# Optimization experiments

Measured on AMD Instinct MI355X. Metric: run time of the kernel, lower is better.

## Reference

```python
import jax, jax.numpy as jnp
import numpy as np

B, A, STATE_LEN, H, REL_LEN, E = 32, 64, 256, 128, 64, 16

def _mlp2(x, w1, b1, w2, b2):
    # DI-engine MLP, 2 layers, ReLU after every layer (incl. output)
    return jax.nn.relu(jax.nn.relu(x @ w1 + b1) @ w2 + b2)

def setup_inputs() -> dict:
    key = jax.random.key(0)
    ks = jax.random.split(key, 16)
    def w(k, fi, fo):
        return (jax.random.normal(k, (fi, fo), jnp.float32) / np.float32(np.sqrt(fi)))
    z = lambda n: jnp.zeros((n,), jnp.float32)
    return {
        "states": jax.random.normal(ks[0], (B, A, STATE_LEN), jnp.float32),
        "relations": jax.random.normal(ks[1], (B, A, A, REL_LEN), jnp.float32),
        "alive_mask": (jax.random.uniform(ks[2], (B, A)) > 0.3).astype(jnp.float32),
        "se_w1": w(ks[3], STATE_LEN, H), "se_b1": z(H),
        "se_w2": w(ks[4], H, H), "se_b2": z(H),
        "re_w1": w(ks[5], H + REL_LEN, H), "re_b1": z(H),
        "re_w2": w(ks[6], H, 2 * H), "re_b2": z(2 * H),
        "ra_w": w(ks[7], 3 * H, H), "ra_b": z(H),
        "ae_w1": w(ks[8], 4 * H, H), "ae_b1": z(H),
        "ae_w2": w(ks[9], H, 2 * H), "ae_b2": z(2 * H),
        "action_embed": jax.random.normal(ks[10], (E, H), jnp.float32) * np.float32(np.sqrt(2.0 / H)),
        "action_mask": jnp.ones((B, A, E + A), jnp.int32),
        "action": jax.random.randint(ks[11], (B,), 0, E + A),
        "agent_id": 0,
    }

def reference(states, relations, alive_mask,
              se_w1, se_b1, se_w2, se_b2,
              re_w1, re_b1, re_w2, re_b2,
              ra_w, ra_b,
              ae_w1, ae_b1, ae_w2, ae_b2,
              action_embed, action_mask, action, agent_id):
    del action_mask  # read by the torch module but never used
    b, a = states.shape[0], states.shape[1]
    h, e = se_w2.shape[1], action_embed.shape[0]
    # encode per-agent state: [B,A,H]
    s = _mlp2(states, se_w1, se_b1, se_w2, se_b2)
    # relation encoder: concat target-agent state onto each relation edge
    rel_in = jnp.concatenate(
        [relations, jnp.broadcast_to(s[:, None], (b, a, a, h))], axis=-1)
    r = _mlp2(rel_in, re_w1, re_b1, re_w2, re_b2)               # [B,A,A,2H]
    # relation aggregator: masked mean / masked max over source agents
    r_avr, r_max = jnp.split(r, 2, axis=-1)
    m = alive_mask[:, None, :, None]                             # [B,1,A,1]
    r_avr = (r_avr * m).mean(axis=-2)                            # [B,A,H]
    r_max = (r_max * m).max(axis=-2)                             # [B,A,H]
    s = jax.nn.relu(jnp.concatenate([s, r_avr, r_max], axis=-1) @ ra_w + ra_b)
    # pairwise action embeddings: [B,A,A,2H]
    ae_in = jnp.concatenate(
        [r,
         jnp.broadcast_to(s[:, None], (b, a, a, h)),
         jnp.broadcast_to(s[:, :, None], (b, a, a, h))], axis=-1)
    ae = _mlp2(ae_in, ae_w1, ae_b1, ae_w2, ae_b2)
    active, passive = jnp.split(ae, 2, axis=-1)                  # [B,A,A,H] each
    # acting agent `agent_id`: candidates = [embed_num self actions | A targeted actions]
    active_i = active[:, agent_id]                               # [B,A,H]
    active_full = jnp.concatenate(
        [jnp.broadcast_to(action_embed[None], (b, e, h)), active_i], axis=1)  # [B,E+A,H]
    sel = jnp.take_along_axis(active_full, action[:, None, None], axis=1)     # [B,1,H]
    state = s.at[:, agent_id].add(sel[:, 0])
    # passive side: target j receives passive embed iff action == E + j, else zero
    passive_i = passive[:, agent_id]                             # [B,A,H]
    hit = (action[:, None] == (e + jnp.arange(a))[None, :])      # [B,A]
    passive_sel = jnp.where(hit[:, :, None], passive_i, jnp.zeros((), states.dtype))
    state = state + passive_sel
    return state, sel[:, :, None], passive_sel
```

## Files before the change

### kernel.cpp

```cpp
#include <hip/hip_runtime.h>

#define NB 32
#define NA 64
#define SLEN 256
#define NH 128
#define RLEN 64
#define NE 16

typedef _Float16 f16;
typedef _Float16 f16x8 __attribute__((ext_vector_type(8)));
typedef _Float16 f16x4 __attribute__((ext_vector_type(4)));
typedef float f32x4 __attribute__((ext_vector_type(4)));

__device__ inline f16x8 cvt8(float4 a, float4 b) {
  f16x8 r;
  r[0] = (f16)a.x; r[1] = (f16)a.y; r[2] = (f16)a.z; r[3] = (f16)a.w;
  r[4] = (f16)b.x; r[5] = (f16)b.y; r[6] = (f16)b.z; r[7] = (f16)b.w;
  return r;
}

__global__ __launch_bounds__(256) void k0_pack(const float* __restrict__ re_w1,
                                               const float* __restrict__ re_w2,
                                               const float* __restrict__ se_w1,
                                               const float* __restrict__ se_w2,
                                               const float* __restrict__ ra_w,
                                               const float* __restrict__ ae_w1,
                                               const float* __restrict__ ae_w2,
                                               f16* __restrict__ pk) {
  int idx = blockIdx.x * 256 + threadIdx.x;
  const float* src;
  int ro, N, ld, base;
  if (idx < 8192)        { src = re_w1; ro = 0;   N = 128; ld = 128; base = 0; }
  else if (idx < 40960)  { src = re_w2; ro = 0;   N = 256; ld = 256; base = 8192; }
  else if (idx < 73728)  { src = se_w1; ro = 0;   N = 128; ld = 128; base = 40960; }
  else if (idx < 90112)  { src = se_w2; ro = 0;   N = 128; ld = 128; base = 73728; }
  else if (idx < 106496) { src = re_w1; ro = 64;  N = 128; ld = 128; base = 90112; }
  else if (idx < 155648) { src = ra_w;  ro = 0;   N = 128; ld = 128; base = 106496; }
  else if (idx < 172032) { src = ae_w1; ro = 256; N = 128; ld = 128; base = 155648; }
  else if (idx < 188416) { src = ae_w1; ro = 384; N = 128; ld = 128; base = 172032; }
  else if (idx < 221184) { src = ae_w1; ro = 0;   N = 128; ld = 128; base = 188416; }
  else if (idx < 253952) { src = ae_w2; ro = 0;   N = 256; ld = 256; base = 221184; }
  else return;
  int li = idx - base;
  int t = li & 7, l = (li >> 3) & 63, rem = li >> 9;
  int NT = N >> 4;
  int nt = rem % NT, kt = rem / NT;
  int k = kt * 32 + (l >> 4) * 8 + t;
  int n = nt * 16 + (l & 15);
  pk[idx] = (f16)src[(size_t)(ro + k) * ld + n];
}

__global__ __launch_bounds__(256) void k1m(const float* __restrict__ states,
                                           const float* __restrict__ se_b1,
                                           const float* __restrict__ se_b2,
                                           const float* __restrict__ re_b1,
                                           const f16* __restrict__ pse1,
                                           const f16* __restrict__ pse2,
                                           const f16* __restrict__ pre1b,
                                           float* __restrict__ s_out,
                                           float* __restrict__ sp_pk) {
  __shared__ f16 t1[16 * 128];
  __shared__ f16 t2[16 * 128];
  const int row0 = blockIdx.x * 16;
  const int tid = threadIdx.x;
  const int w = tid >> 6, l = tid & 63, lr = l & 15, lh = l >> 4;

  f32x4 acc[2];
  acc[0] = (f32x4){0.f, 0.f, 0.f, 0.f};
  acc[1] = (f32x4){0.f, 0.f, 0.f, 0.f};

#pragma unroll
  for (int kt = 0; kt < 8; ++kt) {
    const float* p = states + (size_t)(row0 + lr) * SLEN + kt * 32 + lh * 8;
    f16x8 aF = cvt8(*(const float4*)p, *(const float4*)(p + 4));
#pragma unroll
    for (int n = 0; n < 2; ++n) {
      f16x8 bF = *(const f16x8*)(pse1 + ((size_t)(kt * 8 + w * 2 + n) * 64 + l) * 8);
      acc[n] = __builtin_amdgcn_mfma_f32_16x16x32_f16(aF, bF, acc[n], 0, 0, 0);
    }
  }
#pragma unroll
  for (int n = 0; n < 2; ++n) {
    int h = w * 32 + n * 16 + lr;
    float bias = se_b1[h];
#pragma unroll
    for (int reg = 0; reg < 4; ++reg) {
      int j = lh * 4 + reg;
      float v = fmaxf(acc[n][reg] + bias, 0.f);
      unsigned off = (unsigned)((j * NH + h) * 2) ^ ((unsigned)(j & 7) << 4);
      *(f16*)((char*)t1 + off) = (f16)v;
    }
  }
  __syncthreads();

  acc[0] = (f32x4){0.f, 0.f, 0.f, 0.f};
  acc[1] = (f32x4){0.f, 0.f, 0.f, 0.f};
#pragma unroll
  for (int kt = 0; kt < 4; ++kt) {
    unsigned off = (unsigned)((lr * NH + kt * 32 + lh * 8) * 2) ^ ((unsigned)(lr & 7) << 4);
    f16x8 aF = *(const f16x8*)((char*)t1 + off);
#pragma unroll
    for (int n = 0; n < 2; ++n) {
      f16x8 bF = *(const f16x8*)(pse2 + ((size_t)(kt * 8 + w * 2 + n) * 64 + l) * 8);
      acc[n] = __builtin_amdgcn_mfma_f32_16x16x32_f16(aF, bF, acc[n], 0, 0, 0);
    }
  }
#pragma unroll
  for (int n = 0; n < 2; ++n) {
    int h = w * 32 + n * 16 + lr;
    float bias = se_b2[h];
#pragma unroll
    for (int reg = 0; reg < 4; ++reg) {
      int j = lh * 4 + reg;
      float v = fmaxf(acc[n][reg] + bias, 0.f);
      s_out[(size_t)(row0 + j) * NH + h] = v;
      unsigned off = (unsigned)((j * NH + h) * 2) ^ ((unsigned)(j & 7) << 4);
      *(f16*)((char*)t2 + off) = (f16)v;
    }
  }
  __syncthreads();

  acc[0] = (f32x4){0.f, 0.f, 0.f, 0.f};
  acc[1] = (f32x4){0.f, 0.f, 0.f, 0.f};
#pragma unroll
  for (int kt = 0; kt < 4; ++kt) {
    unsigned off = (unsigned)((lr * NH + kt * 32 + lh * 8) * 2) ^ ((unsigned)(lr & 7) << 4);
    f16x8 aF = *(const f16x8*)((char*)t2 + off);
#pragma unroll
    for (int n = 0; n < 2; ++n) {
      f16x8 bF = *(const f16x8*)(pre1b + ((size_t)(kt * 8 + w * 2 + n) * 64 + l) * 8);
      acc[n] = __builtin_amdgcn_mfma_f32_16x16x32_f16(aF, bF, acc[n], 0, 0, 0);
    }
  }
  const int bb = row0 >> 6;
  const int mtile = (row0 & 63) >> 4;
#pragma unroll
  for (int n = 0; n < 2; ++n) {
    int h = w * 32 + n * 16 + lr;
    float bias = re_b1[h];
    float4 outv;
#pragma unroll
    for (int reg = 0; reg < 4; ++reg) outv[reg] = acc[n][reg] + bias;
    *(float4*)(sp_pk + ((size_t)((bb * 4 + mtile) * 8 + w * 2 + n) * 64 + l) * 4) = outv;
  }
}

__global__ __launch_bounds__(256) void k3_rel(const float* __restrict__ relations,
                                              const float* __restrict__ alive_mask,
                                              const float* __restrict__ sp_pk,
                                              const float* __restrict__ re_b2,
                                              const f16* __restrict__ pw1,
                                              const f16* __restrict__ pw2,
                                              const int* __restrict__ agent_id,
                                              float* __restrict__ r_red,
                                              f16* __restrict__ r_agent) {
  __shared__ f16 tl[64 * 128];
  __shared__ float alive[NA];
  const int bid = blockIdx.x;
  const int b = bid >> 6, i = bid & 63;
  const int tid = threadIdx.x;
  const int w = tid >> 6, l = tid & 63, lr = l & 15, lh = l >> 4;

  if (tid < 64) alive[tid] = alive_mask[b * NA + tid];
  float bz[4];
#pragma unroll
  for (int n = 0; n < 4; ++n) bz[n] = re_b2[w * 64 + n * 16 + lr];

  const float* relp = relations + (size_t)bid * NA * RLEN;
  f16x8 a1[4][2];
#pragma unroll
  for (int mt = 0; mt < 4; ++mt)
#pragma unroll
    for (int kt = 0; kt < 2; ++kt) {
      const float* p = relp + (mt * 16 + lr) * RLEN + kt * 32 + lh * 8;
      a1[mt][kt] = cvt8(*(const float4*)p, *(const float4*)(p + 4));
    }
  f16x8 b1f[2][2];
#pragma unroll
  for (int kt = 0; kt < 2; ++kt)
#pragma unroll
    for (int n = 0; n < 2; ++n)
      b1f[kt][n] = *(const f16x8*)(pw1 + ((size_t)(kt * 8 + w * 2 + n) * 64 + l) * 8);
  float4 sp4[4][2];
  {
    const float* spp = sp_pk + (size_t)b * 8192;
#pragma unroll
    for (int mt = 0; mt < 4; ++mt)
#pragma unroll
      for (int n = 0; n < 2; ++n)
        sp4[mt][n] = *(const float4*)(spp + (size_t)((mt * 8 + w * 2 + n) * 64 + l) * 4);
  }

  f32x4 acc1[4][2];
#pragma unroll
  for (int mt = 0; mt < 4; ++mt)
#pragma unroll
    for (int n = 0; n < 2; ++n) acc1[mt][n] = (f32x4){0.f, 0.f, 0.f, 0.f};
#pragma unroll
  for (int kt = 0; kt < 2; ++kt)
#pragma unroll
    for (int mt = 0; mt < 4; ++mt)
#pragma unroll
      for (int n = 0; n < 2; ++n)
        acc1[mt][n] = __builtin_amdgcn_mfma_f32_16x16x32_f16(a1[mt][kt], b1f[kt][n],
                                                             acc1[mt][n], 0, 0, 0);

#pragma unroll
  for (int mt = 0; mt < 4; ++mt)
#pragma unroll
    for (int n = 0; n < 2; ++n) {
      int h = w * 32 + n * 16 + lr;
#pragma unroll
      for (int reg = 0; reg < 4; ++reg) {
        int j = mt * 16 + lh * 4 + reg;
        float v = fmaxf(acc1[mt][n][reg] + sp4[mt][n][reg], 0.f);
        unsigned off = (unsigned)((j * NH + h) * 2) ^ ((unsigned)(j & 7) << 4);
        *(f16*)((char*)tl + off) = (f16)v;
      }
    }
  __syncthreads();

  f32x4 acc2[4][4];
#pragma unroll
  for (int mt = 0; mt < 4; ++mt)
#pragma unroll
    for (int n = 0; n < 4; ++n) acc2[mt][n] = (f32x4){0.f, 0.f, 0.f, 0.f};
#pragma unroll
  for (int kt2 = 0; kt2 < 4; ++kt2) {
    f16x8 a2[4];
#pragma unroll
    for (int mt = 0; mt < 4; ++mt) {
      int row = mt * 16 + lr;
      unsigned off = (unsigned)((row * 256 + kt2 * 64 + lh * 16)) ^ ((unsigned)(row & 7) << 4);
      a2[mt] = *(const f16x8*)((char*)tl + off);
    }
    f16x8 b2f[4];
#pragma unroll
    for (int n = 0; n < 4; ++n)
      b2f[n] = *(const f16x8*)(pw2 + ((size_t)(kt2 * 16 + w * 4 + n) * 64 + l) * 8);
#pragma unroll
    for (int mt = 0; mt < 4; ++mt)
#pragma unroll
      for (int n = 0; n < 4; ++n)
        acc2[mt][n] = __builtin_amdgcn_mfma_f32_16x16x32_f16(a2[mt], b2f[n], acc2[mt][n], 0, 0, 0);
  }

  const int aid = agent_id[0];
  const bool isagent = (i == aid);
  const bool domax = (w >= 2);
  float red[4];
#pragma unroll
  for (int n = 0; n < 4; ++n) red[n] = 0.f;
#pragma unroll
  for (int n = 0; n < 4; ++n) {
    int col = w * 64 + n * 16 + lr;
    float bias = bz[n];
#pragma unroll
    for (int mt = 0; mt < 4; ++mt)
#pragma unroll
      for (int reg = 0; reg < 4; ++reg) {
        int j = mt * 16 + lh * 4 + reg;
        float rv = fmaxf(acc2[mt][n][reg] + bias, 0.f);
        float rm = rv * alive[j];
        red[n] = domax ? fmaxf(red[n], rm) : (red[n] + rm);
        if (isagent) r_agent[((size_t)b * NA + j) * 256 + col] = (f16)rv;
      }
  }
#pragma unroll
  for (int n = 0; n < 4; ++n) {
    float v = red[n];
    float v1 = __shfl_xor(v, 16, 64);
    v = domax ? fmaxf(v, v1) : v + v1;
    float v2 = __shfl_xor(v, 32, 64);
    v = domax ? fmaxf(v, v2) : v + v2;
    if (lh == 0) r_red[(size_t)bid * 256 + w * 64 + n * 16 + lr] = v;
  }
}

__global__ __launch_bounds__(256) void k4m(const float* __restrict__ s,
                                           const float* __restrict__ r_red,
                                           const float* __restrict__ ra_b,
                                           const f16* __restrict__ pra,
                                           const f16* __restrict__ pae1b,
                                           const f16* __restrict__ pae1c,
                                           float* __restrict__ s_new,
                                           float* __restrict__ sproj2,
                                           float* __restrict__ sproj3) {
  __shared__ f16 x3[16 * 384];
  __shared__ f16 t2[16 * 128];
  const int row0 = blockIdx.x * 16;
  const int tid = threadIdx.x;
  const int w = tid >> 6, l = tid & 63, lr = l & 15, lh = l >> 4;

#pragma unroll
  for (int it = 0; it < 6; ++it) {
    int e = it * 1024 + tid * 4;
    int row = e / 384;
    int c = e - row * 384;
    float4 v;
    if (c < 128) {
      v = *(const float4*)(s + (size_t)(row0 + row) * NH + c);
    } else {
      v = *(const float4*)(r_red + (size_t)(row0 + row) * 256 + (c - 128));
      if (c < 256) { v.x *= (1.f / 64.f); v.y *= (1.f / 64.f); v.z *= (1.f / 64.f); v.w *= (1.f / 64.f); }
    }
    f16x4 hv;
    hv[0] = (f16)v.x; hv[1] = (f16)v.y; hv[2] = (f16)v.z; hv[3] = (f16)v.w;
    unsigned off = (unsigned)((row * 384 + c) * 2) ^ ((unsigned)(row & 7) << 4);
    *(f16x4*)((char*)x3 + off) = hv;
  }
  __syncthreads();

  f32x4 acc[2];
  acc[0] = (f32x4){0.f, 0.f, 0.f, 0.f};
  acc[1] = (f32x4){0.f, 0.f, 0.f, 0.f};
#pragma unroll
  for (int kt = 0; kt < 12; ++kt) {
    unsigned off = (unsigned)((lr * 384 + kt * 32 + lh * 8) * 2) ^ ((unsigned)(lr & 7) << 4);
    f16x8 aF = *(const f16x8*)((char*)x3 + off);
#pragma unroll
    for (int n = 0; n < 2; ++n) {
      f16x8 bF = *(const f16x8*)(pra + ((size_t)(kt * 8 + w * 2 + n) * 64 + l) * 8);
      acc[n] = __builtin_amdgcn_mfma_f32_16x16x32_f16(aF, bF, acc[n], 0, 0, 0);
    }
  }
#pragma unroll
  for (int n = 0; n < 2; ++n) {
    int h = w * 32 + n * 16 + lr;
    float bias = ra_b[h];
#pragma unroll
    for (int reg = 0; reg < 4; ++reg) {
      int j = lh * 4 + reg;
      float v = fmaxf(acc[n][reg] + bias, 0.f);
      s_new[(size_t)(row0 + j) * NH + h] = v;
      unsigned off = (unsigned)((j * NH + h) * 2) ^ ((unsigned)(j & 7) << 4);
      *(f16*)((char*)t2 + off) = (f16)v;
    }
  }
  __syncthreads();

  f32x4 p2[2], p3[2];
  p2[0] = p2[1] = (f32x4){0.f, 0.f, 0.f, 0.f};
  p3[0] = p3[1] = (f32x4){0.f, 0.f, 0.f, 0.f};
#pragma unroll
  for (int kt = 0; kt < 4; ++kt) {
    unsigned off = (unsigned)((lr * NH + kt * 32 + lh * 8) * 2) ^ ((unsigned)(lr & 7) << 4);
    f16x8 aF = *(const f16x8*)((char*)t2 + off);
#pragma unroll
    for (int n = 0; n < 2; ++n) {
      f16x8 b2 = *(const f16x8*)(pae1b + ((size_t)(kt * 8 + w * 2 + n) * 64 + l) * 8);
      f16x8 b3 = *(const f16x8*)(pae1c + ((size_t)(kt * 8 + w * 2 + n) * 64 + l) * 8);
      p2[n] = __builtin_amdgcn_mfma_f32_16x16x32_f16(aF, b2, p2[n], 0, 0, 0);
      p3[n] = __builtin_amdgcn_mfma_f32_16x16x32_f16(aF, b3, p3[n], 0, 0, 0);
    }
  }
#pragma unroll
  for (int n = 0; n < 2; ++n) {
    int h = w * 32 + n * 16 + lr;
#pragma unroll
    for (int reg = 0; reg < 4; ++reg) {
      int j = lh * 4 + reg;
      sproj2[(size_t)(row0 + j) * NH + h] = p2[n][reg];
      sproj3[(size_t)(row0 + j) * NH + h] = p3[n][reg];
    }
  }
}

__global__ __launch_bounds__(256) void kae(const f16* __restrict__ r_agent,
                                           const float* __restrict__ sproj2,
                                           const float* __restrict__ sproj3,
                                           const float* __restrict__ ae_b1,
                                           const float* __restrict__ ae_b2,
                                           const f16* __restrict__ pae1a,
                                           const f16* __restrict__ pae2,
                                           const int* __restrict__ agent_id,
                                           float* __restrict__ ae_full) {
  __shared__ f16 t1[16 * 128];
  const int row0 = blockIdx.x * 16;
  const int b = row0 >> 6;
  const int tid = threadIdx.x;
  const int w = tid >> 6, l = tid & 63, lr = l & 15, lh = l >> 4;
  const int aid = agent_id[0];

  f32x4 acc[2];
  acc[0] = (f32x4){0.f, 0.f, 0.f, 0.f};
  acc[1] = (f32x4){0.f, 0.f, 0.f, 0.f};
#pragma unroll
  for (int kt = 0; kt < 8; ++kt) {
    f16x8 aF = *(const f16x8*)(r_agent + (size_t)(row0 + lr) * 256 + kt * 32 + lh * 8);
#pragma unroll
    for (int n = 0; n < 2; ++n) {
      f16x8 bF = *(const f16x8*)(pae1a + ((size_t)(kt * 8 + w * 2 + n) * 64 + l) * 8);
      acc[n] = __builtin_amdgcn_mfma_f32_16x16x32_f16(aF, bF, acc[n], 0, 0, 0);
    }
  }
#pragma unroll
  for (int n = 0; n < 2; ++n) {
    int h = w * 32 + n * 16 + lr;
    float base = ae_b1[h] + sproj3[((size_t)b * NA + aid) * NH + h];
#pragma unroll
    for (int reg = 0; reg < 4; ++reg) {
      int j = lh * 4 + reg;
      float v = fmaxf(acc[n][reg] + base + sproj2[(size_t)(row0 + j) * NH + h], 0.f);
      unsigned off = (unsigned)((j * NH + h) * 2) ^ ((unsigned)(j & 7) << 4);
      *(f16*)((char*)t1 + off) = (f16)v;
    }
  }
  __syncthreads();

  f32x4 acc2[4];
#pragma unroll
  for (int n = 0; n < 4; ++n) acc2[n] = (f32x4){0.f, 0.f, 0.f, 0.f};
#pragma unroll
  for (int kt = 0; kt < 4; ++kt) {
    unsigned off = (unsigned)((lr * NH + kt * 32 + lh * 8) * 2) ^ ((unsigned)(lr & 7) << 4);
    f16x8 aF = *(const f16x8*)((char*)t1 + off);
#pragma unroll
    for (int n = 0; n < 4; ++n) {
      f16x8 bF = *(const f16x8*)(pae2 + ((size_t)(kt * 16 + w * 4 + n) * 64 + l) * 8);
      acc2[n] = __builtin_amdgcn_mfma_f32_16x16x32_f16(aF, bF, acc2[n], 0, 0, 0);
    }
  }
#pragma unroll
  for (int n = 0; n < 4; ++n) {
    int col = w * 64 + n * 16 + lr;
    float bias = ae_b2[col];
#pragma unroll
    for (int reg = 0; reg < 4; ++reg) {
      int j = lh * 4 + reg;
      ae_full[(size_t)(row0 + j) * 256 + col] = fmaxf(acc2[n][reg] + bias, 0.f);
    }
  }
}

__global__ __launch_bounds__(256) void k5g(const float* __restrict__ action_embed,
                                           const int* __restrict__ action,
                                           const int* __restrict__ agent_id,
                                           const float* __restrict__ ae_full,
                                           const float* __restrict__ s_new,
                                           float* __restrict__ out_state,
                                           float* __restrict__ out_sel,
                                           float* __restrict__ out_passive) {
  __shared__ float selL[128], pasL[128];
  const int b = blockIdx.x;
  const int tid = threadIdx.x;
  const int h = tid & 127;
  const int act = action[b];
  const int aid = agent_id[0];

  if (tid < 128) {
    float sv, pv;
    if (act < NE) {
      sv = action_embed[act * NH + h];
      pv = 0.f;
    } else {
      size_t r = (size_t)(b * NA + act - NE) * 256;
      sv = ae_full[r + h];
      pv = ae_full[r + 128 + h];
    }
    selL[h] = sv;
    pasL[h] = pv;
    out_sel[b * NH + h] = sv;
  }
  __syncthreads();

  const int prow = (act >= NE) ? (act - NE) : -1;
#pragma unroll
  for (int it = 0; it < 8; ++it) {
    int q = it * 256 + tid;
    int i = q >> 5;
    int c = (q & 31) * 4;
    size_t idx = ((size_t)b * NA + i) * NH + c;
    float4 st = *(const float4*)(s_new + idx);
    float4 ps = {0.f, 0.f, 0.f, 0.f};
    if (i == prow) {
      ps.x = pasL[c]; ps.y = pasL[c + 1]; ps.z = pasL[c + 2]; ps.w = pasL[c + 3];
      st.x += ps.x; st.y += ps.y; st.z += ps.z; st.w += ps.w;
    }
    if (i == aid) {
      st.x += selL[c]; st.y += selL[c + 1]; st.z += selL[c + 2]; st.w += selL[c + 3];
    }
    *(float4*)(out_state + idx) = st;
    *(float4*)(out_passive + idx) = ps;
  }
}

extern "C" void kernel_launch(void* const* d_in, const int* in_sizes, int n_in,
                              void* d_out, int out_size, void* d_ws, size_t ws_size,
                              hipStream_t stream) {
  (void)in_sizes; (void)n_in; (void)out_size; (void)ws_size;
  const float* states       = (const float*)d_in[0];
  const float* relations    = (const float*)d_in[1];
  const float* alive_mask   = (const float*)d_in[2];
  const float* se_w1        = (const float*)d_in[3];
  const float* se_b1        = (const float*)d_in[4];
  const float* se_w2        = (const float*)d_in[5];
  const float* se_b2        = (const float*)d_in[6];
  const float* re_w1        = (const float*)d_in[7];
  const float* re_b1        = (const float*)d_in[8];
  const float* re_w2        = (const float*)d_in[9];
  const float* re_b2        = (const float*)d_in[10];
  const float* ra_w         = (const float*)d_in[11];
  const float* ra_b         = (const float*)d_in[12];
  const float* ae_w1        = (const float*)d_in[13];
  const float* ae_b1        = (const float*)d_in[14];
  const float* ae_w2        = (const float*)d_in[15];
  const float* ae_b2        = (const float*)d_in[16];
  const float* action_embed = (const float*)d_in[17];
  const int*   action       = (const int*)d_in[19];
  const int*   agent_id     = (const int*)d_in[20];
  float* out = (float*)d_out;

  float* wsf     = (float*)d_ws;
  float* s       = wsf;
  float* sp_pk   = wsf + 262144;
  float* r_red   = wsf + 524288;
  float* s_new   = wsf + 1048576;
  float* sproj2  = wsf + 1310720;
  float* sproj3  = wsf + 1572864;
  float* ae_full = wsf + 1835008;
  f16*   wsh     = (f16*)(wsf + 2359296);
  f16*   r_agent = wsh;
  f16*   pk      = wsh + 524288;
  f16*   pw_re1a = pk;
  f16*   pw_re2  = pk + 8192;
  f16*   pw_se1  = pk + 40960;
  f16*   pw_se2  = pk + 73728;
  f16*   pw_re1b = pk + 90112;
  f16*   pw_ra   = pk + 106496;
  f16*   pw_ae1b = pk + 155648;
  f16*   pw_ae1c = pk + 172032;
  f16*   pw_ae1a = pk + 188416;
  f16*   pw_ae2  = pk + 221184;

  k0_pack<<<992, 256, 0, stream>>>(re_w1, re_w2, se_w1, se_w2, ra_w, ae_w1, ae_w2, pk);
  k1m<<<128, 256, 0, stream>>>(states, se_b1, se_b2, re_b1, pw_se1, pw_se2, pw_re1b,
                               s, sp_pk);
  k3_rel<<<2048, 256, 0, stream>>>(relations, alive_mask, sp_pk, re_b2, pw_re1a, pw_re2,
                                   agent_id, r_red, r_agent);
  k4m<<<128, 256, 0, stream>>>(s, r_red, ra_b, pw_ra, pw_ae1b, pw_ae1c,
                               s_new, sproj2, sproj3);
  kae<<<128, 256, 0, stream>>>(r_agent, sproj2, sproj3, ae_b1, ae_b2, pw_ae1a, pw_ae2,
                               agent_id, ae_full);
  k5g<<<32, 256, 0, stream>>>(action_embed, action, agent_id, ae_full, s_new,
                              out, out + 262144, out + 266240);
}
```

Baseline: 167.6 us.

## Compute action MLP only for selected rows and pipeline relation loads

The relation kernel now handles four source agents per block and prefetches each next relations tile into double-buffered LDS with async global-to-LDS loads, overlapping the load with the MFMA work. The action-embedding MLP is evaluated only for the one selected target row per batch (32 rows) rather than all 2048 agent pairs, and the sproj precompute in k4m is folded into a single 512-wide GEMM input. The final scatter kernel becomes a flat elementwise pass. The cost is fewer blocks in the relation kernel (512) and a tiny two-block MLP kernel that runs serially.

New measurement: 168.1 us. No clear change (+0.3%).

```diff
diff --git a/kernel.cpp b/kernel.cpp
--- a/kernel.cpp
+++ b/kernel.cpp
@@ -17,6 +17,11 @@
   r[0] = (f16)a.x; r[1] = (f16)a.y; r[2] = (f16)a.z; r[3] = (f16)a.w;
   r[4] = (f16)b.x; r[5] = (f16)b.y; r[6] = (f16)b.z; r[7] = (f16)b.w;
   return r;
+}
+
+__device__ inline void gload_lds16(const float* g, float* l) {
+  __builtin_amdgcn_global_load_lds((const __attribute__((address_space(1))) void*)g,
+                                   (__attribute__((address_space(3))) void*)l, 16, 0, 0);
 }
 
 __global__ __launch_bounds__(256) void k0_pack(const float* __restrict__ re_w1,
@@ -154,27 +159,30 @@
                                               const int* __restrict__ agent_id,
                                               float* __restrict__ r_red,
                                               f16* __restrict__ r_agent) {
+  __shared__ float relb[2][64 * 64];
   __shared__ f16 tl[64 * 128];
   __shared__ float alive[NA];
   const int bid = blockIdx.x;
-  const int b = bid >> 6, i = bid & 63;
+  const int b = bid >> 4;
+  const int i0 = (bid & 15) * 4;
   const int tid = threadIdx.x;
   const int w = tid >> 6, l = tid & 63, lr = l & 15, lh = l >> 4;
 
+  auto stage = [&](int buf, int i) {
+    const float* g = relations + (size_t)(b * NA + i) * NA * RLEN;
+#pragma unroll
+    for (int c4 = 0; c4 < 4; ++c4) {
+      int c = w * 4 + c4;
+      int srcf = c * 256 + ((l ^ ((4 * c + (l >> 4)) & 7)) * 4);
+      gload_lds16(g + srcf, &relb[buf][c * 256]);
+    }
+  };
+
+  stage(0, i0);
   if (tid < 64) alive[tid] = alive_mask[b * NA + tid];
   float bz[4];
 #pragma unroll
   for (int n = 0; n < 4; ++n) bz[n] = re_b2[w * 64 + n * 16 + lr];
-
-  const float* relp = relations + (size_t)bid * NA * RLEN;
-  f16x8 a1[4][2];
-#pragma unroll
-  for (int mt = 0; mt < 4; ++mt)
-#pragma unroll
-    for (int kt = 0; kt < 2; ++kt) {
-      const float* p = relp + (mt * 16 + lr) * RLEN + kt * 32 + lh * 8;
-      a1[mt][kt] = cvt8(*(const float4*)p, *(const float4*)(p + 4));
-    }
   f16x8 b1f[2][2];
 #pragma unroll
   for (int kt = 0; kt < 2; ++kt)
@@ -190,90 +198,108 @@
       for (int n = 0; n < 2; ++n)
         sp4[mt][n] = *(const float4*)(spp + (size_t)((mt * 8 + w * 2 + n) * 64 + l) * 4);
   }
-
-  f32x4 acc1[4][2];
-#pragma unroll
-  for (int mt = 0; mt < 4; ++mt)
-#pragma unroll
-    for (int n = 0; n < 2; ++n) acc1[mt][n] = (f32x4){0.f, 0.f, 0.f, 0.f};
-#pragma unroll
-  for (int kt = 0; kt < 2; ++kt)
+  const int aid = agent_id[0];
+  const bool domax = (w >= 2);
+  __syncthreads();
+
+  for (int t = 0; t < 4; ++t) {
+    const int cur = t & 1;
+    f32x4 acc1[4][2];
 #pragma unroll
     for (int mt = 0; mt < 4; ++mt)
 #pragma unroll
-      for (int n = 0; n < 2; ++n)
-        acc1[mt][n] = __builtin_amdgcn_mfma_f32_16x16x32_f16(a1[mt][kt], b1f[kt][n],
-                                                             acc1[mt][n], 0, 0, 0);
-
-#pragma unroll
-  for (int mt = 0; mt < 4; ++mt)
-#pragma unroll
-    for (int n = 0; n < 2; ++n) {
-      int h = w * 32 + n * 16 + lr;
-#pragma unroll
-      for (int reg = 0; reg < 4; ++reg) {
-        int j = mt * 16 + lh * 4 + reg;
-        float v = fmaxf(acc1[mt][n][reg] + sp4[mt][n][reg], 0.f);
-        unsigned off = (unsigned)((j * NH + h) * 2) ^ ((unsigned)(j & 7) << 4);
-        *(f16*)((char*)tl + off) = (f16)v;
+      for (int n = 0; n < 2; ++n) acc1[mt][n] = (f32x4){0.f, 0.f, 0.f, 0.f};
+#pragma unroll
+    for (int mt = 0; mt < 4; ++mt) {
+      int R = mt * 16 + lr;
+      unsigned sw = ((unsigned)(R & 7)) << 4;
+      f16x8 aK[2];
+#pragma unroll
+      for (int kt = 0; kt < 2; ++kt) {
+        unsigned base = (unsigned)((R * 64 + kt * 32 + lh * 8) * 4);
+        float4 v0 = *(const float4*)((char*)relb[cur] + (base ^ sw));
+        float4 v1 = *(const float4*)((char*)relb[cur] + ((base + 16) ^ sw));
+        aK[kt] = cvt8(v0, v1);
       }
-    }
-  __syncthreads();
-
-  f32x4 acc2[4][4];
-#pragma unroll
-  for (int mt = 0; mt < 4; ++mt)
-#pragma unroll
-    for (int n = 0; n < 4; ++n) acc2[mt][n] = (f32x4){0.f, 0.f, 0.f, 0.f};
-#pragma unroll
-  for (int kt2 = 0; kt2 < 4; ++kt2) {
-    f16x8 a2[4];
-#pragma unroll
-    for (int mt = 0; mt < 4; ++mt) {
-      int row = mt * 16 + lr;
-      unsigned off = (unsigned)((row * 256 + kt2 * 64 + lh * 16)) ^ ((unsigned)(row & 7) << 4);
-      a2[mt] = *(const f16x8*)((char*)tl + off);
-    }
-    f16x8 b2f[4];
-#pragma unroll
-    for (int n = 0; n < 4; ++n)
-      b2f[n] = *(const f16x8*)(pw2 + ((size_t)(kt2 * 16 + w * 4 + n) * 64 + l) * 8);
+#pragma unroll
+      for (int kt = 0; kt < 2; ++kt)
+#pragma unroll
+        for (int n = 0; n < 2; ++n)
+          acc1[mt][n] = __builtin_amdgcn_mfma_f32_16x16x32_f16(aK[kt], b1f[kt][n],
+                                                               acc1[mt][n], 0, 0, 0);
+    }
 #pragma unroll
     for (int mt = 0; mt < 4; ++mt)
 #pragma unroll
+      for (int n = 0; n < 2; ++n) {
+        int h = w * 32 + n * 16 + lr;
+#pragma unroll
+        for (int reg = 0; reg < 4; ++reg) {
+          int j = mt * 16 + lh * 4 + reg;
+          float v = fmaxf(acc1[mt][n][reg] + sp4[mt][n][reg], 0.f);
+          unsigned off = (unsigned)((j * NH + h) * 2) ^ ((unsigned)(j & 7) << 4);
+          *(f16*)((char*)tl + off) = (f16)v;
+        }
+      }
+    __syncthreads();
+
+    if (t < 3) stage(cur ^ 1, i0 + t + 1);
+
+    f32x4 acc2[4][4];
+#pragma unroll
+    for (int mt = 0; mt < 4; ++mt)
+#pragma unroll
+      for (int n = 0; n < 4; ++n) acc2[mt][n] = (f32x4){0.f, 0.f, 0.f, 0.f};
+#pragma unroll
+    for (int kt2 = 0; kt2 < 4; ++kt2) {
+      f16x8 a2[4];
+#pragma unroll
+      for (int mt = 0; mt < 4; ++mt) {
+        int row = mt * 16 + lr;
+        unsigned off = (unsigned)((row * 256 + kt2 * 64 + lh * 16)) ^ ((unsigned)(row & 7) << 4);
+        a2[mt] = *(const f16x8*)((char*)tl + off);
+      }
+      f16x8 b2f[4];
+#pragma unroll
       for (int n = 0; n < 4; ++n)
-        acc2[mt][n] = __builtin_amdgcn_mfma_f32_16x16x32_f16(a2[mt], b2f[n], acc2[mt][n], 0, 0, 0);
-  }
-
-  const int aid = agent_id[0];
-  const bool isagent = (i == aid);
-  const bool domax = (w >= 2);
-  float red[4];
-#pragma unroll
-  for (int n = 0; n < 4; ++n) red[n] = 0.f;
-#pragma unroll
-  for (int n = 0; n < 4; ++n) {
-    int col = w * 64 + n * 16 + lr;
-    float bias = bz[n];
-#pragma unroll
-    for (int mt = 0; mt < 4; ++mt)
-#pragma unroll
-      for (int reg = 0; reg < 4; ++reg) {
-        int j = mt * 16 + lh * 4 + reg;
-        float rv = fmaxf(acc2[mt][n][reg] + bias, 0.f);
-        float rm = rv * alive[j];
-        red[n] = domax ? fmaxf(red[n], rm) : (red[n] + rm);
-        if (isagent) r_agent[((size_t)b * NA + j) * 256 + col] = (f16)rv;
-      }
-  }
-#pragma unroll
-  for (int n = 0; n < 4; ++n) {
-    float v = red[n];
-    float v1 = __shfl_xor(v, 16, 64);
-    v = domax ? fmaxf(v, v1) : v + v1;
-    float v2 = __shfl_xor(v, 32, 64);
-    v = domax ? fmaxf(v, v2) : v + v2;
-    if (lh == 0) r_red[(size_t)bid * 256 + w * 64 + n * 16 + lr] = v;
+        b2f[n] = *(const f16x8*)(pw2 + ((size_t)(kt2 * 16 + w * 4 + n) * 64 + l) * 8);
+#pragma unroll
+      for (int mt = 0; mt < 4; ++mt)
+#pragma unroll
+        for (int n = 0; n < 4; ++n)
+          acc2[mt][n] = __builtin_amdgcn_mfma_f32_16x16x32_f16(a2[mt], b2f[n], acc2[mt][n], 0, 0, 0);
+    }
+
+    const int i = i0 + t;
+    const bool isagent = (i == aid);
+    float red[4];
+#pragma unroll
+    for (int n = 0; n < 4; ++n) red[n] = 0.f;
+#pragma unroll
+    for (int n = 0; n < 4; ++n) {
+      int col = w * 64 + n * 16 + lr;
+      float bias = bz[n];
+#pragma unroll
+      for (int mt = 0; mt < 4; ++mt)
+#pragma unroll
+        for (int reg = 0; reg < 4; ++reg) {
+          int j = mt * 16 + lh * 4 + reg;
+          float rv = fmaxf(acc2[mt][n][reg] + bias, 0.f);
+          float rm = rv * alive[j];
+          red[n] = domax ? fmaxf(red[n], rm) : (red[n] + rm);
+          if (isagent) r_agent[((size_t)b * NA + j) * 256 + col] = (f16)rv;
+        }
+    }
+#pragma unroll
+    for (int n = 0; n < 4; ++n) {
+      float v = red[n];
+      float v1 = __shfl_xor(v, 16, 64);
+      v = domax ? fmaxf(v, v1) : v + v1;
+      float v2 = __shfl_xor(v, 32, 64);
+      v = domax ? fmaxf(v, v2) : v + v2;
+      if (lh == 0) r_red[(size_t)(b * NA + i) * 256 + w * 64 + n * 16 + lr] = v;
+    }
+    __syncthreads();
   }
 }
 
@@ -281,13 +307,8 @@
                                            const float* __restrict__ r_red,
                                            const float* __restrict__ ra_b,
                                            const f16* __restrict__ pra,
-                                           const f16* __restrict__ pae1b,
-                                           const f16* __restrict__ pae1c,
-                                           float* __restrict__ s_new,
-                                           float* __restrict__ sproj2,
-                                           float* __restrict__ sproj3) {
+                                           float* __restrict__ s_new) {
   __shared__ f16 x3[16 * 384];
-  __shared__ f16 t2[16 * 128];
   const int row0 = blockIdx.x * 16;
   const int tid = threadIdx.x;
   const int w = tid >> 6, l = tid & 63, lr = l & 15, lh = l >> 4;
@@ -331,77 +352,83 @@
 #pragma unroll
     for (int reg = 0; reg < 4; ++reg) {
       int j = lh * 4 + reg;
-      float v = fmaxf(acc[n][reg] + bias, 0.f);
-      s_new[(size_t)(row0 + j) * NH + h] = v;
-      unsigned off = (unsigned)((j * NH + h) * 2) ^ ((unsigned)(j & 7) << 4);
-      *(f16*)((char*)t2 + off) = (f16)v;
-    }
-  }
-  __syncthreads();
-
-  f32x4 p2[2], p3[2];
-  p2[0] = p2[1] = (f32x4){0.f, 0.f, 0.f, 0.f};
-  p3[0] = p3[1] = (f32x4){0.f, 0.f, 0.f, 0.f};
-#pragma unroll
-  for (int kt = 0; kt < 4; ++kt) {
-    unsigned off = (unsigned)((lr * NH + kt * 32 + lh * 8) * 2) ^ ((unsigned)(lr & 7) << 4);
-    f16x8 aF = *(const f16x8*)((char*)t2 + off);
-#pragma unroll
-    for (int n = 0; n < 2; ++n) {
-      f16x8 b2 = *(const f16x8*)(pae1b + ((size_t)(kt * 8 + w * 2 + n) * 64 + l) * 8);
-      f16x8 b3 = *(const f16x8*)(pae1c + ((size_t)(kt * 8 + w * 2 + n) * 64 + l) * 8);
-      p2[n] = __builtin_amdgcn_mfma_f32_16x16x32_f16(aF, b2, p2[n], 0, 0, 0);
-      p3[n] = __builtin_amdgcn_mfma_f32_16x16x32_f16(aF, b3, p3[n], 0, 0, 0);
-    }
-  }
-#pragma unroll
-  for (int n = 0; n < 2; ++n) {
-    int h = w * 32 + n * 16 + lr;
-#pragma unroll
-    for (int reg = 0; reg < 4; ++reg) {
-      int j = lh * 4 + reg;
-      sproj2[(size_t)(row0 + j) * NH + h] = p2[n][reg];
-      sproj3[(size_t)(row0 + j) * NH + h] = p3[n][reg];
-    }
-  }
-}
-
-__global__ __launch_bounds__(256) void kae(const f16* __restrict__ r_agent,
-                                           const float* __restrict__ sproj2,
-                                           const float* __restrict__ sproj3,
+      s_new[(size_t)(row0 + j) * NH + h] = fmaxf(acc[n][reg] + bias, 0.f);
+    }
+  }
+}
+
+__global__ __launch_bounds__(256) void k5m(const f16* __restrict__ r_agent,
+                                           const float* __restrict__ s_new,
                                            const float* __restrict__ ae_b1,
                                            const float* __restrict__ ae_b2,
+                                           const float* __restrict__ action_embed,
+                                           const int* __restrict__ action,
+                                           const int* __restrict__ agent_id,
                                            const f16* __restrict__ pae1a,
+                                           const f16* __restrict__ pae1b,
+                                           const f16* __restrict__ pae1c,
                                            const f16* __restrict__ pae2,
-                                           const int* __restrict__ agent_id,
-                                           float* __restrict__ ae_full) {
+                                           float* __restrict__ sel_ws,
+                                           float* __restrict__ pas_ws,
+                                           float* __restrict__ out_sel) {
+  __shared__ f16 xa[16 * 512];
   __shared__ f16 t1[16 * 128];
-  const int row0 = blockIdx.x * 16;
-  const int b = row0 >> 6;
+  __shared__ int actL[16];
+  const int b0 = blockIdx.x * 16;
   const int tid = threadIdx.x;
   const int w = tid >> 6, l = tid & 63, lr = l & 15, lh = l >> 4;
   const int aid = agent_id[0];
 
+  {
+    int row = tid & 15, g = tid >> 4;
+    int bb = b0 + row;
+    int act = action[bb];
+    if (g == 0) actL[row] = act;
+    int jj = act >= NE ? act - NE : 0;
+    int k0 = g * 32;
+    f16x8 vv[4];
+    if (g < 8) {
+      const f16* src = r_agent + ((size_t)bb * NA + jj) * 256 + k0;
+#pragma unroll
+      for (int c = 0; c < 4; ++c) vv[c] = *(const f16x8*)(src + c * 8);
+    } else {
+      const float* src = (g < 12) ? (s_new + ((size_t)bb * NA + jj) * NH + (g - 8) * 32)
+                                  : (s_new + ((size_t)bb * NA + aid) * NH + (g - 12) * 32);
+#pragma unroll
+      for (int c = 0; c < 4; ++c)
+        vv[c] = cvt8(*(const float4*)(src + c * 8), *(const float4*)(src + c * 8 + 4));
+    }
+#pragma unroll
+    for (int c = 0; c < 4; ++c) {
+      unsigned off = (unsigned)((row * 512 + k0 + c * 8) * 2) ^ ((unsigned)(row & 7) << 4);
+      *(f16x8*)((char*)xa + off) = vv[c];
+    }
+  }
+  __syncthreads();
+
   f32x4 acc[2];
   acc[0] = (f32x4){0.f, 0.f, 0.f, 0.f};
   acc[1] = (f32x4){0.f, 0.f, 0.f, 0.f};
 #pragma unroll
-  for (int kt = 0; kt < 8; ++kt) {
-    f16x8 aF = *(const f16x8*)(r_agent + (size_t)(row0 + lr) * 256 + kt * 32 + lh * 8);
+  for (int kt = 0; kt < 16; ++kt) {
+    unsigned off = (unsigned)((lr * 512 + kt * 32 + lh * 8) * 2) ^ ((unsigned)(lr & 7) << 4);
+    f16x8 aF = *(const f16x8*)((char*)xa + off);
+    const f16* pseg = (kt < 8) ? pae1a : (kt < 12) ? pae1b : pae1c;
+    int ktl = (kt < 8) ? kt : (kt < 12) ? kt - 8 : kt - 12;
 #pragma unroll
     for (int n = 0; n < 2; ++n) {
-      f16x8 bF = *(const f16x8*)(pae1a + ((size_t)(kt * 8 + w * 2 + n) * 64 + l) * 8);
+      f16x8 bF = *(const f16x8*)(pseg + ((size_t)(ktl * 8 + w * 2 + n) * 64 + l) * 8);
       acc[n] = __builtin_amdgcn_mfma_f32_16x16x32_f16(aF, bF, acc[n], 0, 0, 0);
     }
   }
 #pragma unroll
   for (int n = 0; n < 2; ++n) {
     int h = w * 32 + n * 16 + lr;
-    float base = ae_b1[h] + sproj3[((size_t)b * NA + aid) * NH + h];
+    float bias = ae_b1[h];
 #pragma unroll
     for (int reg = 0; reg < 4; ++reg) {
       int j = lh * 4 + reg;
-      float v = fmaxf(acc[n][reg] + base + sproj2[(size_t)(row0 + j) * NH + h], 0.f);
+      float v = fmaxf(acc[n][reg] + bias, 0.f);
       unsigned off = (unsigned)((j * NH + h) * 2) ^ ((unsigned)(j & 7) << 4);
       *(f16*)((char*)t1 + off) = (f16)v;
     }
@@ -427,62 +454,47 @@
     float bias = ae_b2[col];
 #pragma unroll
     for (int reg = 0; reg < 4; ++reg) {
-      int j = lh * 4 + reg;
-      ae_full[(size_t)(row0 + j) * 256 + col] = fmaxf(acc2[n][reg] + bias, 0.f);
-    }
-  }
-}
-
-__global__ __launch_bounds__(256) void k5g(const float* __restrict__ action_embed,
-                                           const int* __restrict__ action,
+      int row = lh * 4 + reg;
+      int bb = b0 + row;
+      int act = actL[row];
+      float v = fmaxf(acc2[n][reg] + bias, 0.f);
+      if (col < NH) {
+        float sv = (act < NE) ? action_embed[act * NH + col] : v;
+        sel_ws[bb * NH + col] = sv;
+        out_sel[bb * NH + col] = sv;
+      } else {
+        pas_ws[bb * NH + col - NH] = (act < NE) ? 0.f : v;
+      }
+    }
+  }
+}
+
+__global__ __launch_bounds__(256) void k5g(const int* __restrict__ action,
                                            const int* __restrict__ agent_id,
-                                           const float* __restrict__ ae_full,
+                                           const float* __restrict__ sel_ws,
+                                           const float* __restrict__ pas_ws,
                                            const float* __restrict__ s_new,
                                            float* __restrict__ out_state,
-                                           float* __restrict__ out_sel,
                                            float* __restrict__ out_passive) {
-  __shared__ float selL[128], pasL[128];
-  const int b = blockIdx.x;
-  const int tid = threadIdx.x;
-  const int h = tid & 127;
-  const int act = action[b];
-  const int aid = agent_id[0];
-
-  if (tid < 128) {
-    float sv, pv;
-    if (act < NE) {
-      sv = action_embed[act * NH + h];
-      pv = 0.f;
-    } else {
-      size_t r = (size_t)(b * NA + act - NE) * 256;
-      sv = ae_full[r + h];
-      pv = ae_full[r + 128 + h];
-    }
-    selL[h] = sv;
-    pasL[h] = pv;
-    out_sel[b * NH + h] = sv;
-  }
-  __syncthreads();
-
-  const int prow = (act >= NE) ? (act - NE) : -1;
-#pragma unroll
-  for (int it = 0; it < 8; ++it) {
-    int q = it * 256 + tid;
-    int i = q >> 5;
-    int c = (q & 31) * 4;
-    size_t idx = ((size_t)b * NA + i) * NH + c;
-    float4 st = *(const float4*)(s_new + idx);
-    float4 ps = {0.f, 0.f, 0.f, 0.f};
-    if (i == prow) {
-      ps.x = pasL[c]; ps.y = pasL[c + 1]; ps.z = pasL[c + 2]; ps.w = pasL[c + 3];
-      st.x += ps.x; st.y += ps.y; st.z += ps.z; st.w += ps.w;
-    }
-    if (i == aid) {
-      st.x += selL[c]; st.y += selL[c + 1]; st.z += selL[c + 2]; st.w += selL[c + 3];
-    }
-    *(float4*)(out_state + idx) = st;
-    *(float4*)(out_passive + idx) = ps;
-  }
+  int q = blockIdx.x * 256 + threadIdx.x;
+  int idx = q * 4;
+  int h = idx & 127;
+  int row = idx >> 7;
+  int b = row >> 6, i = row & 63;
+  int act = action[b];
+  int aid = agent_id[0];
+  float4 st = *(const float4*)(s_new + idx);
+  float4 ps = {0.f, 0.f, 0.f, 0.f};
+  if (act >= NE && i == act - NE) {
+    ps = *(const float4*)(pas_ws + b * NH + h);
+    st.x += ps.x; st.y += ps.y; st.z += ps.z; st.w += ps.w;
+  }
+  if (i == aid) {
+    const float4 sl = *(const float4*)(sel_ws + b * NH + h);
+    st.x += sl.x; st.y += sl.y; st.z += sl.z; st.w += sl.w;
+  }
+  *(float4*)(out_state + idx) = st;
+  *(float4*)(out_passive + idx) = ps;
 }
 
 extern "C" void kernel_launch(void* const* d_in, const int* in_sizes, int n_in,
@@ -516,10 +528,9 @@
   float* sp_pk   = wsf + 262144;
   float* r_red   = wsf + 524288;
   float* s_new   = wsf + 1048576;
-  float* sproj2  = wsf + 1310720;
-  float* sproj3  = wsf + 1572864;
-  float* ae_full = wsf + 1835008;
-  f16*   wsh     = (f16*)(wsf + 2359296);
+  float* sel_ws  = wsf + 1310720;
+  float* pas_ws  = wsf + 1314816;
+  f16*   wsh     = (f16*)(wsf + 1318912);
   f16*   r_agent = wsh;
   f16*   pk      = wsh + 524288;
   f16*   pw_re1a = pk;
@@ -536,12 +547,12 @@
   k0_pack<<<992, 256, 0, stream>>>(re_w1, re_w2, se_w1, se_w2, ra_w, ae_w1, ae_w2, pk);
   k1m<<<128, 256, 0, stream>>>(states, se_b1, se_b2, re_b1, pw_se1, pw_se2, pw_re1b,
                                s, sp_pk);
-  k3_rel<<<2048, 256, 0, stream>>>(relations, alive_mask, sp_pk, re_b2, pw_re1a, pw_re2,
-                                   agent_id, r_red, r_agent);
-  k4m<<<128, 256, 0, stream>>>(s, r_red, ra_b, pw_ra, pw_ae1b, pw_ae1c,
-                               s_new, sproj2, sproj3);
-  kae<<<128, 256, 0, stream>>>(r_agent, sproj2, sproj3, ae_b1, ae_b2, pw_ae1a, pw_ae2,
-                               agent_id, ae_full);
-  k5g<<<32, 256, 0, stream>>>(action_embed, action, agent_id, ae_full, s_new,
-                              out, out + 262144, out + 266240);
-}
+  k3_rel<<<512, 256, 0, stream>>>(relations, alive_mask, sp_pk, re_b2, pw_re1a, pw_re2,
+                                  agent_id, r_red, r_agent);
+  k4m<<<128, 256, 0, stream>>>(s, r_red, ra_b, pw_ra, s_new);
+  k5m<<<2, 256, 0, stream>>>(r_agent, s_new, ae_b1, ae_b2, action_embed, action,
+                             agent_id, pw_ae1a, pw_ae1b, pw_ae1c, pw_ae2,
+                             sel_ws, pas_ws, out + 262144);
+  k5g<<<256, 256, 0, stream>>>(action, agent_id, sel_ws, pas_ws, s_new,
+                               out, out + 266240);
+}
```
